# Optimization experiments

Hardware: AMD Instinct MI355X
Metric: run time of the kernel (lower is better)

## Reference

```python
import jax, jax.numpy as jnp
import numpy as np

N_NODES = 50000
N_EDGES = 800000
HIDDEN = 128
OUT = 10
N_LAYERS = 2
N_GRAPHS = 128
EPS = 1e-5


def setup_inputs() -> dict:
    key = jax.random.key(0)
    ks = jax.random.split(key, 10)
    x = jax.random.normal(ks[0], (N_NODES, HIDDEN), dtype=jnp.float32)
    edge_index = jax.random.randint(ks[1], (2, N_EDGES), 0, N_NODES, dtype=jnp.int64)
    batch = jnp.sort(jax.random.randint(ks[2], (N_NODES,), 0, N_GRAPHS, dtype=jnp.int64))
    s = 1.0 / np.sqrt(HIDDEN)
    # GraphConv params per layer: lin_rel (weight+bias, applied to aggregated neighbors)
    # and lin_root (weight, applied to the node itself). LayerNorm gamma/beta per layer.
    W_rel = jax.random.uniform(ks[3], (N_LAYERS, HIDDEN, HIDDEN), jnp.float32, -s, s)
    b_rel = jax.random.uniform(ks[4], (N_LAYERS, HIDDEN), jnp.float32, -s, s)
    W_root = jax.random.uniform(ks[5], (N_LAYERS, HIDDEN, HIDDEN), jnp.float32, -s, s)
    gamma = jnp.ones((N_LAYERS, HIDDEN), jnp.float32)
    beta = jnp.zeros((N_LAYERS, HIDDEN), jnp.float32)
    Wc = jax.random.uniform(ks[6], (HIDDEN, OUT), jnp.float32, -s, s)
    bc = jax.random.uniform(ks[7], (OUT,), jnp.float32, -s, s)
    return {"x": x, "edge_index": edge_index, "batch": batch,
            "W_rel": W_rel, "b_rel": b_rel, "W_root": W_root,
            "gamma": gamma, "beta": beta, "Wc": Wc, "bc": bc}


def _layer_norm(x, g, b):
    mu = jnp.mean(x, axis=-1, keepdims=True)
    var = jnp.mean(jnp.square(x - mu), axis=-1, keepdims=True)
    return g * (x - mu) * jax.lax.rsqrt(var + EPS) + b


def reference(x, edge_index, batch, W_rel, b_rel, W_root, gamma, beta, Wc, bc):
    src, dst = edge_index[0], edge_index[1]
    n = x.shape[0]
    # in-degree for mean aggregation (PyG: zero rows for isolated nodes)
    deg = jax.ops.segment_sum(jnp.ones((src.shape[0],), x.dtype), dst, num_segments=n)
    inv_deg = jnp.where(deg > 0, 1.0 / jnp.maximum(deg, 1.0), 0.0)[:, None]
    for l in range(N_LAYERS):
        agg = jax.ops.segment_sum(x[src], dst, num_segments=n) * inv_deg  # [N, H]
        x = agg @ W_rel[l] + b_rel[l] + x @ W_root[l]
        x = _layer_norm(x, gamma[l], beta[l])
        x = jax.nn.relu(x)
        # feat_dropout = 0.0 -> identity
    cnt = jax.ops.segment_sum(jnp.ones((n,), x.dtype), batch, num_segments=N_GRAPHS)
    pooled = jax.ops.segment_sum(x, batch, num_segments=N_GRAPHS)
    pooled = pooled / jnp.maximum(cnt, 1.0)[:, None]  # [G, H]
    return pooled @ Wc + bc
```

## Files before the change

### kernel.cpp

```cpp
#include <hip/hip_runtime.h>
#include <hip/hip_bf16.h>

#define N_NODES 50000
#define N_EDGES 800000
#define HIDDEN  128
#define OUT_F   10
#define N_GRAPHS 128
#define EPS 1e-5f

#define NB   391
#define BCAP 3072
#define SLICE (N_EDGES / 256)

#define CASTX_BLOCKS 12500
#define CASTW_BLOCKS 256
#define POOLZ_BLOCKS 64

using short8 = __attribute__((ext_vector_type(8))) short;
using f32x4  = __attribute__((ext_vector_type(4))) float;

__global__ void cast_zero_kernel(const float* __restrict__ x, __hip_bfloat16* __restrict__ xb,
                                 const float* __restrict__ Wrel, const float* __restrict__ Wroot,
                                 __hip_bfloat16* __restrict__ Wt,
                                 int* __restrict__ cursor, float* __restrict__ pooled) {
    const int b = blockIdx.x, tid = threadIdx.x;
    if (b < CASTX_BLOCKS) {
        int i = b * 256 + tid;
        float2 v = ((const float2*)x)[i];
        __hip_bfloat162 o;
        o.x = __float2bfloat16(v.x);
        o.y = __float2bfloat16(v.y);
        ((__hip_bfloat162*)xb)[i] = o;
    } else if (b < CASTX_BLOCKS + CASTW_BLOCKS) {
        int idx = (b - CASTX_BLOCKS) * 256 + tid;
        int l = idx >> 15;
        int rem = idx & 32767;
        int n = rem >> 8;
        int k = rem & 255;
        float v = (k < HIDDEN) ? Wrel[l * HIDDEN * HIDDEN + k * HIDDEN + n]
                               : Wroot[l * HIDDEN * HIDDEN + (k - HIDDEN) * HIDDEN + n];
        Wt[idx] = __float2bfloat16(v);
    } else if (b < CASTX_BLOCKS + CASTW_BLOCKS + POOLZ_BLOCKS) {
        int i = (b - CASTX_BLOCKS - CASTW_BLOCKS) * 256 + tid;
        pooled[i] = 0.f;
    } else {
        for (int i = tid; i < NB; i += 256) cursor[i] = 0;
    }
}

__global__ __launch_bounds__(256) void part_kernel(
        const int* __restrict__ src, const int* __restrict__ dst,
        int* __restrict__ cursor, int* __restrict__ ebuf) {
    __shared__ int s_pk[SLICE];
    __shared__ unsigned short s_bk[SLICE];
    __shared__ int hist[NB], base[NB];
    const int tid = threadIdx.x;
    const int e0 = blockIdx.x * SLICE;
    for (int i = tid; i < NB; i += 256) hist[i] = 0;
    __syncthreads();
    for (int i = tid; i < SLICE; i += 256) {
        int s = src[e0 + i], d = dst[e0 + i];
        int b = d >> 7;
        s_pk[i] = s | ((d & 127) << 16);
        s_bk[i] = (unsigned short)b;
        atomicAdd(&hist[b], 1);
    }
    __syncthreads();
    for (int i = tid; i < NB; i += 256) {
        int h = hist[i];
        base[i] = h ? atomicAdd(&cursor[i], h) : 0;
        hist[i] = 0;
    }
    __syncthreads();
    for (int i = tid; i < SLICE; i += 256) {
        int b = s_bk[i];
        int off = base[b] + atomicAdd(&hist[b], 1);
        if (off < BCAP) ebuf[b * BCAP + off] = s_pk[i];
    }
}

__global__ __launch_bounds__(256) void fillb_kernel(
        const int* __restrict__ cursor, const int* __restrict__ ebuf,
        int* __restrict__ row_ptr, float* __restrict__ inv_deg,
        int* __restrict__ csr_src) {
    __shared__ int lcsr[BCAP];
    __shared__ int hist[128], lofs[128];
    __shared__ int wtot[2];
    __shared__ int sred[4];
    __shared__ int sbase;
    const int b = blockIdx.x;
    const int tid = threadIdx.x;

    int partial = 0;
    for (int i = tid; i < b; i += 256) partial += cursor[i];
    #pragma unroll
    for (int off = 1; off < 64; off <<= 1) partial += __shfl_xor(partial, off, 64);
    if ((tid & 63) == 0) sred[tid >> 6] = partial;
    if (tid < 128) hist[tid] = 0;
    __syncthreads();
    if (tid == 0) sbase = sred[0] + sred[1] + sred[2] + sred[3];
    __syncthreads();
    const int base = sbase;

    int cnt = cursor[b]; if (cnt > BCAP) cnt = BCAP;
    const int* eb = ebuf + b * BCAP;

    for (int i = tid; i < cnt; i += 256) atomicAdd(&hist[eb[i] >> 16], 1);
    __syncthreads();
    if (tid < 128) {
        int lane = tid & 63;
        int v = hist[tid];
        int inc = v;
        #pragma unroll
        for (int off = 1; off < 64; off <<= 1) {
            int t = __shfl_up(inc, off, 64);
            if (lane >= off) inc += t;
        }
        lofs[tid] = inc - v;
        if (lane == 63) wtot[tid >> 6] = inc;
    }
    __syncthreads();
    if (tid >= 64 && tid < 128) lofs[tid] += wtot[0];
    __syncthreads();
    if (tid < 128) {
        int node = b * 128 + tid;
        if (node < N_NODES) {
            row_ptr[node] = base + lofs[tid];
            int d = hist[tid];
            inv_deg[node] = (d > 0) ? (1.0f / (float)d) : 0.0f;
        }
        hist[tid] = lofs[tid];
    }
    if (b == 0 && tid == 0) row_ptr[N_NODES] = N_EDGES;
    __syncthreads();
    for (int i = tid; i < cnt; i += 256) {
        int pk = eb[i];
        int p = atomicAdd(&hist[pk >> 16], 1);
        lcsr[p] = pk & 0xFFFF;
    }
    __syncthreads();
    for (int i = tid; i < cnt; i += 256) csr_src[base + i] = lcsr[i];
}

__global__ void agg_kernel(const __hip_bfloat16* __restrict__ x, const int* __restrict__ row_ptr,
                           const int* __restrict__ csr_src, const float* __restrict__ inv_deg,
                           __hip_bfloat16* __restrict__ agg) {
    int gid = blockIdx.x * blockDim.x + threadIdx.x;
    int node = gid >> 6;
    int lane = threadIdx.x & 63;
    if (node >= N_NODES) return;
    const int half = lane >> 5;
    const int l32  = lane & 31;
    const int beg = row_ptr[node], end = row_ptr[node + 1];

    float a[4][4];
    #pragma unroll
    for (int u = 0; u < 4; ++u)
        #pragma unroll
        for (int k = 0; k < 4; ++k) a[u][k] = 0.f;

    for (int c = beg; c < end; c += 64) {
        int ei = c + lane;
        int sidx = (ei < end) ? csr_src[ei] : 0;
        int nedge = end - c; if (nedge > 64) nedge = 64;
        int npair = nedge >> 1;
        int j = 0;
        for (; j + 4 <= npair; j += 4) {
            #pragma unroll
            for (int u = 0; u < 4; ++u) {
                int sj = __shfl(sidx, 2 * (j + u) + half, 64);
                float2 v = ((const float2*)(x + (size_t)sj * HIDDEN))[l32];
                __hip_bfloat162 b0 = *(__hip_bfloat162*)&v.x;
                __hip_bfloat162 b1 = *(__hip_bfloat162*)&v.y;
                a[u][0] += __bfloat162float(b0.x);
                a[u][1] += __bfloat162float(b0.y);
                a[u][2] += __bfloat162float(b1.x);
                a[u][3] += __bfloat162float(b1.y);
            }
        }
        for (; j < npair; ++j) {
            int sj = __shfl(sidx, 2 * j + half, 64);
            float2 v = ((const float2*)(x + (size_t)sj * HIDDEN))[l32];
            __hip_bfloat162 b0 = *(__hip_bfloat162*)&v.x;
            __hip_bfloat162 b1 = *(__hip_bfloat162*)&v.y;
            a[0][0] += __bfloat162float(b0.x);
            a[0][1] += __bfloat162float(b0.y);
            a[0][2] += __bfloat162float(b1.x);
            a[0][3] += __bfloat162float(b1.y);
        }
        if (nedge & 1) {
            int sj = __shfl(sidx, nedge - 1, 64);
            if (half == 0) {
                float2 v = ((const float2*)(x + (size_t)sj * HIDDEN))[l32];
                __hip_bfloat162 b0 = *(__hip_bfloat162*)&v.x;
                __hip_bfloat162 b1 = *(__hip_bfloat162*)&v.y;
                a[0][0] += __bfloat162float(b0.x);
                a[0][1] += __bfloat162float(b0.y);
                a[0][2] += __bfloat162float(b1.x);
                a[0][3] += __bfloat162float(b1.y);
            }
        }
    }

    float s0 = a[0][0] + a[1][0] + a[2][0] + a[3][0];
    float s1 = a[0][1] + a[1][1] + a[2][1] + a[3][1];
    float s2 = a[0][2] + a[1][2] + a[2][2] + a[3][2];
    float s3 = a[0][3] + a[1][3] + a[2][3] + a[3][3];
    s0 += __shfl_xor(s0, 32, 64);
    s1 += __shfl_xor(s1, 32, 64);
    s2 += __shfl_xor(s2, 32, 64);
    s3 += __shfl_xor(s3, 32, 64);

    if (half == 0) {
        float w = inv_deg[node];
        __hip_bfloat162 p0, p1;
        p0.x = __float2bfloat16(s0 * w);
        p0.y = __float2bfloat16(s1 * w);
        p1.x = __float2bfloat16(s2 * w);
        p1.y = __float2bfloat16(s3 * w);
        __hip_bfloat162* op = (__hip_bfloat162*)agg + (size_t)node * 64 + l32 * 2;
        op[0] = p0;
        op[1] = p1;
    }
}

#define GM 64

__global__ __launch_bounds__(256) void gemm_mfma_ln_kernel(
        const __hip_bfloat16* __restrict__ aggb, const __hip_bfloat16* __restrict__ xb,
        __hip_bfloat16* __restrict__ xout,
        const __hip_bfloat16* __restrict__ Wt,
        const float* __restrict__ brel, const float* __restrict__ gamma,
        const float* __restrict__ beta) {
    __shared__ __align__(16) short sA[GM * 264];
    __shared__ float red[GM][4][2];

    const int tid  = threadIdx.x;
    const int w    = tid >> 6;
    const int lane = tid & 63;
    const int q    = lane >> 4;
    const int l15  = lane & 15;
    const int base = blockIdx.x * GM;

    short8 breg[2][8];
    #pragma unroll
    for (int nt = 0; nt < 2; ++nt) {
        int col = 32 * w + nt * 16 + l15;
        const short* wp = (const short*)Wt + (size_t)col * 256;
        #pragma unroll
        for (int ks = 0; ks < 8; ++ks)
            breg[nt][ks] = *(const short8*)(wp + ks * 32 + q * 8);
    }

    for (int it = 0; it < 8; ++it) {
        int c = it * 256 + tid;
        int row = c >> 5, cc = c & 31;
        int node = base + row;
        short8 v = {0,0,0,0,0,0,0,0};
        if (node < N_NODES) {
            const short* gp = (cc < 16)
                ? (const short*)aggb + (size_t)node * HIDDEN + cc * 8
                : (const short*)xb   + (size_t)node * HIDDEN + (cc - 16) * 8;
            v = *(const short8*)gp;
        }
        *(short8*)&sA[row * 264 + cc * 8] = v;
    }
    __syncthreads();

    f32x4 acc[4][2];
    #pragma unroll
    for (int mt = 0; mt < 4; ++mt)
        #pragma unroll
        for (int nt = 0; nt < 2; ++nt)
            acc[mt][nt] = (f32x4){0.f, 0.f, 0.f, 0.f};

    #pragma unroll
    for (int ks = 0; ks < 8; ++ks) {
        short8 a[4];
        #pragma unroll
        for (int mt = 0; mt < 4; ++mt)
            a[mt] = *(short8*)&sA[(mt * 16 + l15) * 264 + ks * 32 + q * 8];
        #pragma unroll
        for (int mt = 0; mt < 4; ++mt) {
            acc[mt][0] = __builtin_amdgcn_mfma_f32_16x16x32_bf16(a[mt], breg[0][ks], acc[mt][0], 0, 0, 0);
            acc[mt][1] = __builtin_amdgcn_mfma_f32_16x16x32_bf16(a[mt], breg[1][ks], acc[mt][1], 0, 0, 0);
        }
    }

    const int col0 = 32 * w + l15, col1 = col0 + 16;
    const float b0 = brel[col0], b1 = brel[col1];
    #pragma unroll
    for (int mt = 0; mt < 4; ++mt) {
        #pragma unroll
        for (int r = 0; r < 4; ++r) {
            acc[mt][0][r] += b0;
            acc[mt][1][r] += b1;
            float s  = acc[mt][0][r] + acc[mt][1][r];
            float s2 = acc[mt][0][r] * acc[mt][0][r] + acc[mt][1][r] * acc[mt][1][r];
            #pragma unroll
            for (int off = 1; off < 16; off <<= 1) {
                s  += __shfl_xor(s,  off, 64);
                s2 += __shfl_xor(s2, off, 64);
            }
            if (l15 == 0) {
                red[mt * 16 + q * 4 + r][w][0] = s;
                red[mt * 16 + q * 4 + r][w][1] = s2;
            }
        }
    }
    __syncthreads();

    const float g0 = gamma[col0], g1 = gamma[col1];
    const float e0 = beta[col0],  e1 = beta[col1];
    #pragma unroll
    for (int mt = 0; mt < 4; ++mt) {
        #pragma unroll
        for (int r = 0; r < 4; ++r) {
            int row = mt * 16 + q * 4 + r;
            float tot  = red[row][0][0] + red[row][1][0] + red[row][2][0] + red[row][3][0];
            float tot2 = red[row][0][1] + red[row][1][1] + red[row][2][1] + red[row][3][1];
            float mu  = tot * (1.0f / HIDDEN);
            float var = tot2 * (1.0f / HIDDEN) - mu * mu;
            float rs  = rsqrtf(var + EPS);
            int node = base + row;
            if (node < N_NODES) {
                float v0 = fmaxf(g0 * (acc[mt][0][r] - mu) * rs + e0, 0.f);
                float v1 = fmaxf(g1 * (acc[mt][1][r] - mu) * rs + e1, 0.f);
                xout[(size_t)node * HIDDEN + col0] = __float2bfloat16(v0);
                xout[(size_t)node * HIDDEN + col1] = __float2bfloat16(v1);
            }
        }
    }
}

__global__ __launch_bounds__(256) void gemm_mfma_pool_kernel(
        const __hip_bfloat16* __restrict__ aggb, const __hip_bfloat16* __restrict__ xb,
        const int* __restrict__ batch, float* __restrict__ pooled,
        const __hip_bfloat16* __restrict__ Wt,
        const float* __restrict__ brel, const float* __restrict__ gamma,
        const float* __restrict__ beta) {
    __shared__ __align__(16) short sA[GM * 264];
    __shared__ float red[GM][4][2];
    __shared__ int sbatch[GM];

    const int tid  = threadIdx.x;
    const int w    = tid >> 6;
    const int lane = tid & 63;
    const int q    = lane >> 4;
    const int l15  = lane & 15;
    const int base = blockIdx.x * GM;

    if (tid < GM) {
        int node = base + tid;
        sbatch[tid] = (node < N_NODES) ? batch[node] : -1;
    }

    short8 breg[2][8];
    #pragma unroll
    for (int nt = 0; nt < 2; ++nt) {
        int col = 32 * w + nt * 16 + l15;
        const short* wp = (const short*)Wt + (size_t)col * 256;
        #pragma unroll
        for (int ks = 0; ks < 8; ++ks)
            breg[nt][ks] = *(const short8*)(wp + ks * 32 + q * 8);
    }

    for (int it = 0; it < 8; ++it) {
        int c = it * 256 + tid;
        int row = c >> 5, cc = c & 31;
        int node = base + row;
        short8 v = {0,0,0,0,0,0,0,0};
        if (node < N_NODES) {
            const short* gp = (cc < 16)
                ? (const short*)aggb + (size_t)node * HIDDEN + cc * 8
                : (const short*)xb   + (size_t)node * HIDDEN + (cc - 16) * 8;
            v = *(const short8*)gp;
        }
        *(short8*)&sA[row * 264 + cc * 8] = v;
    }
    __syncthreads();

    f32x4 acc[4][2];
    #pragma unroll
    for (int mt = 0; mt < 4; ++mt)
        #pragma unroll
        for (int nt = 0; nt < 2; ++nt)
            acc[mt][nt] = (f32x4){0.f, 0.f, 0.f, 0.f};

    #pragma unroll
    for (int ks = 0; ks < 8; ++ks) {
        short8 a[4];
        #pragma unroll
        for (int mt = 0; mt < 4; ++mt)
            a[mt] = *(short8*)&sA[(mt * 16 + l15) * 264 + ks * 32 + q * 8];
        #pragma unroll
        for (int mt = 0; mt < 4; ++mt) {
            acc[mt][0] = __builtin_amdgcn_mfma_f32_16x16x32_bf16(a[mt], breg[0][ks], acc[mt][0], 0, 0, 0);
            acc[mt][1] = __builtin_amdgcn_mfma_f32_16x16x32_bf16(a[mt], breg[1][ks], acc[mt][1], 0, 0, 0);
        }
    }

    const int col0 = 32 * w + l15, col1 = col0 + 16;
    const float b0 = brel[col0], b1 = brel[col1];
    #pragma unroll
    for (int mt = 0; mt < 4; ++mt) {
        #pragma unroll
        for (int r = 0; r < 4; ++r) {
            acc[mt][0][r] += b0;
            acc[mt][1][r] += b1;
            float s  = acc[mt][0][r] + acc[mt][1][r];
            float s2 = acc[mt][0][r] * acc[mt][0][r] + acc[mt][1][r] * acc[mt][1][r];
            #pragma unroll
            for (int off = 1; off < 16; off <<= 1) {
                s  += __shfl_xor(s,  off, 64);
                s2 += __shfl_xor(s2, off, 64);
            }
            if (l15 == 0) {
                red[mt * 16 + q * 4 + r][w][0] = s;
                red[mt * 16 + q * 4 + r][w][1] = s2;
            }
        }
    }
    __syncthreads();

    const float g0 = gamma[col0], g1 = gamma[col1];
    const float e0 = beta[col0],  e1 = beta[col1];
    #pragma unroll
    for (int mt = 0; mt < 4; ++mt) {
        #pragma unroll
        for (int r = 0; r < 4; ++r) {
            int row = mt * 16 + q * 4 + r;
            float tot  = red[row][0][0] + red[row][1][0] + red[row][2][0] + red[row][3][0];
            float tot2 = red[row][0][1] + red[row][1][1] + red[row][2][1] + red[row][3][1];
            float mu  = tot * (1.0f / HIDDEN);
            float var = tot2 * (1.0f / HIDDEN) - mu * mu;
            float rs  = rsqrtf(var + EPS);
            bool valid = (base + row) < N_NODES;
            float v0 = valid ? fmaxf(g0 * (acc[mt][0][r] - mu) * rs + e0, 0.f) : 0.f;
            float v1 = valid ? fmaxf(g1 * (acc[mt][1][r] - mu) * rs + e1, 0.f) : 0.f;
            acc[mt][0][r] = v0;
            acc[mt][1][r] = v1;
        }
    }

    int idxmax = N_NODES - 1 - base; if (idxmax > GM - 1) idxmax = GM - 1;
    const int gmin = sbatch[0], gmax = sbatch[idxmax];
    for (int g = gmin; g <= gmax; ++g) {
        float p0 = 0.f, p1 = 0.f;
        #pragma unroll
        for (int mt = 0; mt < 4; ++mt) {
            #pragma unroll
            for (int r = 0; r < 4; ++r) {
                int row = mt * 16 + q * 4 + r;
                if (sbatch[row] == g) { p0 += acc[mt][0][r]; p1 += acc[mt][1][r]; }
            }
        }
        p0 += __shfl_xor(p0, 16, 64); p0 += __shfl_xor(p0, 32, 64);
        p1 += __shfl_xor(p1, 16, 64); p1 += __shfl_xor(p1, 32, 64);
        if (q == 0) {
            atomicAdd(&pooled[g * HIDDEN + col0], p0);
            atomicAdd(&pooled[g * HIDDEN + col1], p1);
        }
    }
}

__global__ void out_kernel(const float* __restrict__ pooled, const int* __restrict__ batch,
                           const float* __restrict__ Wc, const float* __restrict__ bc,
                           float* __restrict__ out) {
    int idx = blockIdx.x * blockDim.x + threadIdx.x;
    if (idx >= N_GRAPHS * OUT_F) return;
    int g = idx / OUT_F, o = idx % OUT_F;
    int lo = 0, hi = N_NODES;
    while (lo < hi) { int m = (lo + hi) >> 1; if (batch[m] < g) lo = m + 1; else hi = m; }
    int b0 = lo;
    lo = 0; hi = N_NODES;
    while (lo < hi) { int m = (lo + hi) >> 1; if (batch[m] < g + 1) lo = m + 1; else hi = m; }
    float cntf = (float)(lo - b0);
    float inv = 1.0f / fmaxf(cntf, 1.0f);
    float s = 0.f;
    for (int f = 0; f < HIDDEN; ++f)
        s += pooled[g * HIDDEN + f] * Wc[f * OUT_F + o];
    out[idx] = s * inv + bc[o];
}

static inline size_t align256(size_t v) { return (v + 255) & ~(size_t)255; }

extern "C" void kernel_launch(void* const* d_in, const int* in_sizes, int n_in,
                              void* d_out, int out_size, void* d_ws, size_t ws_size,
                              hipStream_t stream) {
    const float* x      = (const float*)d_in[0];
    const int*   eidx   = (const int*)d_in[1];
    const int*   batch  = (const int*)d_in[2];
    const float* W_rel  = (const float*)d_in[3];
    const float* b_rel  = (const float*)d_in[4];
    const float* W_root = (const float*)d_in[5];
    const float* gamma  = (const float*)d_in[6];
    const float* beta   = (const float*)d_in[7];
    const float* Wc     = (const float*)d_in[8];
    const float* bc     = (const float*)d_in[9];
    float* out = (float*)d_out;

    const int* src = eidx;
    const int* dst = eidx + N_EDGES;

    char* ws = (char*)d_ws;
    size_t off = 0;
    int*   row_ptr  = (int*)(ws + off);  off = align256(off + sizeof(int) * (N_NODES + 1));
    int*   csr_src  = (int*)(ws + off);  off = align256(off + sizeof(int) * N_EDGES);
    float* inv_deg  = (float*)(ws + off); off = align256(off + sizeof(float) * N_NODES);
    int*   cursor   = (int*)(ws + off);  off = align256(off + sizeof(int) * NB);
    int*   ebuf     = (int*)(ws + off);  off = align256(off + sizeof(int) * (size_t)NB * BCAP);
    __hip_bfloat16* x0b  = (__hip_bfloat16*)(ws + off); off = align256(off + 2 * (size_t)N_NODES * HIDDEN);
    __hip_bfloat16* x1b  = (__hip_bfloat16*)(ws + off); off = align256(off + 2 * (size_t)N_NODES * HIDDEN);
    __hip_bfloat16* aggb = (__hip_bfloat16*)(ws + off); off = align256(off + 2 * (size_t)N_NODES * HIDDEN);
    __hip_bfloat16* Wt   = (__hip_bfloat16*)(ws + off); off = align256(off + 2 * (size_t)2 * HIDDEN * 256);
    float* pooled   = (float*)(ws + off); off = align256(off + sizeof(float) * N_GRAPHS * HIDDEN);

    cast_zero_kernel<<<CASTX_BLOCKS + CASTW_BLOCKS + POOLZ_BLOCKS + 1, 256, 0, stream>>>(
        x, x0b, W_rel, W_root, Wt, cursor, pooled);

    part_kernel <<<256, 256, 0, stream>>>(src, dst, cursor, ebuf);
    fillb_kernel<<<NB, 256, 0, stream>>>(cursor, ebuf, row_ptr, inv_deg, csr_src);

    const int agg_blocks  = (N_NODES * 64) / 256;
    const int gemm_blocks = (N_NODES + GM - 1) / GM;

    agg_kernel<<<agg_blocks, 256, 0, stream>>>(x0b, row_ptr, csr_src, inv_deg, aggb);
    gemm_mfma_ln_kernel<<<gemm_blocks, 256, 0, stream>>>(
        aggb, x0b, x1b, Wt, b_rel, gamma, beta);
    agg_kernel<<<agg_blocks, 256, 0, stream>>>(x1b, row_ptr, csr_src, inv_deg, aggb);
    gemm_mfma_pool_kernel<<<gemm_blocks, 256, 0, stream>>>(
        aggb, x1b, batch, pooled, Wt + 2 * HIDDEN * 256 / 2,
        b_rel + HIDDEN, gamma + HIDDEN, beta + HIDDEN);

    out_kernel<<<(N_GRAPHS * OUT_F + 255) / 256, 256, 0, stream>>>(pooled, batch, Wc, bc, out);
}
```

Measured before the change: 229.9 us.

## Gather neighbor features in FP8 and merge partition into prep kernel

Adds FP8 (e4m3) copies of the node features, written by the cast kernel and by the layer-1 LayerNorm epilogue. The aggregation kernels gather these instead of the bf16 rows, halving the bytes read per edge in the memory-bound gather. Separately, the edge-partition kernel is merged into the cast/prep launch, and the cursor is zeroed with a memset. The FP8 path loses precision in the aggregated features, which may hurt accuracy tolerance, and the extra byte-wise FP8 stores add write traffic to the GEMM epilogue.

```diff
diff --git a/kernel.cpp b/kernel.cpp
--- a/kernel.cpp
+++ b/kernel.cpp
@@ -1,5 +1,6 @@
 #include <hip/hip_runtime.h>
 #include <hip/hip_bf16.h>
+#include <hip/hip_fp8.h>
 
 #define N_NODES 50000
 #define N_EDGES 800000
@@ -12,27 +13,88 @@
 #define BCAP 3072
 #define SLICE (N_EDGES / 256)
 
-#define CASTX_BLOCKS 12500
-#define CASTW_BLOCKS 256
-#define POOLZ_BLOCKS 64
+#define PART_B0   0
+#define CASTW_B0  256
+#define POOLZ_B0  512
+#define CASTX_B0  576
+#define CASTX_NB  6250
+#define PREP_NB   (CASTX_B0 + CASTX_NB)
 
 using short8 = __attribute__((ext_vector_type(8))) short;
 using f32x4  = __attribute__((ext_vector_type(4))) float;
 
-__global__ void cast_zero_kernel(const float* __restrict__ x, __hip_bfloat16* __restrict__ xb,
-                                 const float* __restrict__ Wrel, const float* __restrict__ Wroot,
-                                 __hip_bfloat16* __restrict__ Wt,
-                                 int* __restrict__ cursor, float* __restrict__ pooled) {
+__device__ __forceinline__ unsigned int f4_to_fp8x4(float a, float b, float c, float d) {
+#if __has_builtin(__builtin_amdgcn_cvt_pk_fp8_f32)
+    int v = 0;
+    v = __builtin_amdgcn_cvt_pk_fp8_f32(a, b, v, false);
+    v = __builtin_amdgcn_cvt_pk_fp8_f32(c, d, v, true);
+    return (unsigned int)v;
+#else
+    __hip_fp8_e4m3 ha(a), hb(b), hc(c), hd(d);
+    return (unsigned int)ha.__x | ((unsigned int)hb.__x << 8) |
+           ((unsigned int)hc.__x << 16) | ((unsigned int)hd.__x << 24);
+#endif
+}
+__device__ __forceinline__ unsigned char f_to_fp8(float a) {
+#if __has_builtin(__builtin_amdgcn_cvt_pk_fp8_f32)
+    return (unsigned char)(__builtin_amdgcn_cvt_pk_fp8_f32(a, a, 0, false) & 0xff);
+#else
+    __hip_fp8_e4m3 h(a); return h.__x;
+#endif
+}
+__device__ __forceinline__ void fp8x4_to_f(unsigned int w, float o[4]) {
+#if __has_builtin(__builtin_amdgcn_cvt_pk_f32_fp8)
+    typedef float v2f __attribute__((ext_vector_type(2)));
+    v2f lo = __builtin_amdgcn_cvt_pk_f32_fp8((int)w, false);
+    v2f hi = __builtin_amdgcn_cvt_pk_f32_fp8((int)w, true);
+    o[0] = lo.x; o[1] = lo.y; o[2] = hi.x; o[3] = hi.y;
+#else
+    #pragma unroll
+    for (int t = 0; t < 4; ++t) {
+        __hip_fp8_e4m3 h; h.__x = (unsigned char)((w >> (8 * t)) & 0xff);
+        o[t] = (float)h;
+    }
+#endif
+}
+
+__global__ __launch_bounds__(256) void prep_kernel(
+        const float* __restrict__ x, __hip_bfloat16* __restrict__ x0b,
+        unsigned char* __restrict__ x0f,
+        const float* __restrict__ Wrel, const float* __restrict__ Wroot,
+        __hip_bfloat16* __restrict__ Wt,
+        const int* __restrict__ src, const int* __restrict__ dst,
+        int* __restrict__ cursor, int* __restrict__ ebuf,
+        float* __restrict__ pooled) {
+    __shared__ int s_pk[SLICE];
+    __shared__ unsigned short s_bk[SLICE];
+    __shared__ int hist[NB], base[NB];
     const int b = blockIdx.x, tid = threadIdx.x;
-    if (b < CASTX_BLOCKS) {
-        int i = b * 256 + tid;
-        float2 v = ((const float2*)x)[i];
-        __hip_bfloat162 o;
-        o.x = __float2bfloat16(v.x);
-        o.y = __float2bfloat16(v.y);
-        ((__hip_bfloat162*)xb)[i] = o;
-    } else if (b < CASTX_BLOCKS + CASTW_BLOCKS) {
-        int idx = (b - CASTX_BLOCKS) * 256 + tid;
+
+    if (b < CASTW_B0) {
+        const int e0 = b * SLICE;
+        for (int i = tid; i < NB; i += 256) hist[i] = 0;
+        __syncthreads();
+        for (int i = tid; i < SLICE; i += 256) {
+            int s = src[e0 + i], d = dst[e0 + i];
+            int bk = d >> 7;
+            s_pk[i] = s | ((d & 127) << 16);
+            s_bk[i] = (unsigned short)bk;
+            atomicAdd(&hist[bk], 1);
+        }
+        __syncthreads();
+        for (int i = tid; i < NB; i += 256) {
+            int h = hist[i];
+            base[i] = h ? atomicAdd(&cursor[i], h) : 0;
+            hist[i] = 0;
+        }
+        __syncthreads();
+        for (int i = tid; i < SLICE; i += 256) {
+            int bk = s_bk[i];
+            int off = base[bk] + atomicAdd(&hist[bk], 1);
+            if (off < BCAP) ebuf[bk * BCAP + off] = s_pk[i];
+        }
+    } else if (b < POOLZ_B0) {
+        int idx = (b - CASTW_B0) * 256 + tid;
         int l = idx >> 15;
         int rem = idx & 32767;
         int n = rem >> 8;
@@ -40,42 +102,19 @@
         float v = (k < HIDDEN) ? Wrel[l * HIDDEN * HIDDEN + k * HIDDEN + n]
                                : Wroot[l * HIDDEN * HIDDEN + (k - HIDDEN) * HIDDEN + n];
         Wt[idx] = __float2bfloat16(v);
-    } else if (b < CASTX_BLOCKS + CASTW_BLOCKS + POOLZ_BLOCKS) {
-        int i = (b - CASTX_BLOCKS - CASTW_BLOCKS) * 256 + tid;
+    } else if (b < CASTX_B0) {
+        int i = (b - POOLZ_B0) * 256 + tid;
         pooled[i] = 0.f;
     } else {
-        for (int i = tid; i < NB; i += 256) cursor[i] = 0;
-    }
-}
-
-__global__ __launch_bounds__(256) void part_kernel(
-        const int* __restrict__ src, const int* __restrict__ dst,
-        int* __restrict__ cursor, int* __restrict__ ebuf) {
-    __shared__ int s_pk[SLICE];
-    __shared__ unsigned short s_bk[SLICE];
-    __shared__ int hist[NB], base[NB];
-    const int tid = threadIdx.x;
-    const int e0 = blockIdx.x * SLICE;
-    for (int i = tid; i < NB; i += 256) hist[i] = 0;
-    __syncthreads();
-    for (int i = tid; i < SLICE; i += 256) {
-        int s = src[e0 + i], d = dst[e0 + i];
-        int b = d >> 7;
-        s_pk[i] = s | ((d & 127) << 16);
-        s_bk[i] = (unsigned short)b;
-        atomicAdd(&hist[b], 1);
-    }
-    __syncthreads();
-    for (int i = tid; i < NB; i += 256) {
-        int h = hist[i];
-        base[i] = h ? atomicAdd(&cursor[i], h) : 0;
-        hist[i] = 0;
-    }
-    __syncthreads();
-    for (int i = tid; i < SLICE; i += 256) {
-        int b = s_bk[i];
-        int off = base[b] + atomicAdd(&hist[b], 1);
-        if (off < BCAP) ebuf[b * BCAP + off] = s_pk[i];
+        int i = (b - CASTX_B0) * 256 + tid;
+        float4 v = ((const float4*)x)[i];
+        union { __hip_bfloat162 h[2]; uint2 u; } o;
+        o.h[0].x = __float2bfloat16(v.x);
+        o.h[0].y = __float2bfloat16(v.y);
+        o.h[1].x = __float2bfloat16(v.z);
+        o.h[1].y = __float2bfloat16(v.w);
+        ((uint2*)x0b)[i] = o.u;
+        ((unsigned int*)x0f)[i] = f4_to_fp8x4(v.x, v.y, v.z, v.w);
     }
 }
 
@@ -142,7 +181,7 @@
     for (int i = tid; i < cnt; i += 256) csr_src[base + i] = lcsr[i];
 }
 
-__global__ void agg_kernel(const __hip_bfloat16* __restrict__ x, const int* __restrict__ row_ptr,
+__global__ void agg_kernel(const unsigned char* __restrict__ xf8, const int* __restrict__ row_ptr,
                            const int* __restrict__ csr_src, const float* __restrict__ inv_deg,
                            __hip_bfloat16* __restrict__ agg) {
     int gid = blockIdx.x * blockDim.x + threadIdx.x;
@@ -169,35 +208,26 @@
             #pragma unroll
             for (int u = 0; u < 4; ++u) {
                 int sj = __shfl(sidx, 2 * (j + u) + half, 64);
-                float2 v = ((const float2*)(x + (size_t)sj * HIDDEN))[l32];
-                __hip_bfloat162 b0 = *(__hip_bfloat162*)&v.x;
-                __hip_bfloat162 b1 = *(__hip_bfloat162*)&v.y;
-                a[u][0] += __bfloat162float(b0.x);
-                a[u][1] += __bfloat162float(b0.y);
-                a[u][2] += __bfloat162float(b1.x);
-                a[u][3] += __bfloat162float(b1.y);
+                unsigned int wv = ((const unsigned int*)(xf8 + (size_t)sj * HIDDEN))[l32];
+                float f[4];
+                fp8x4_to_f(wv, f);
+                a[u][0] += f[0]; a[u][1] += f[1]; a[u][2] += f[2]; a[u][3] += f[3];
             }
         }
         for (; j < npair; ++j) {
             int sj = __shfl(sidx, 2 * j + half, 64);
-            float2 v = ((const float2*)(x + (size_t)sj * HIDDEN))[l32];
-            __hip_bfloat162 b0 = *(__hip_bfloat162*)&v.x;
-            __hip_bfloat162 b1 = *(__hip_bfloat162*)&v.y;
-            a[0][0] += __bfloat162float(b0.x);
-            a[0][1] += __bfloat162float(b0.y);
-            a[0][2] += __bfloat162float(b1.x);
-            a[0][3] += __bfloat162float(b1.y);
+            unsigned int wv = ((const unsigned int*)(xf8 + (size_t)sj * HIDDEN))[l32];
+            float f[4];
+            fp8x4_to_f(wv, f);
+            a[0][0] += f[0]; a[0][1] += f[1]; a[0][2] += f[2]; a[0][3] += f[3];
         }
         if (nedge & 1) {
             int sj = __shfl(sidx, nedge - 1, 64);
             if (half == 0) {
-                float2 v = ((const float2*)(x + (size_t)sj * HIDDEN))[l32];
-                __hip_bfloat162 b0 = *(__hip_bfloat162*)&v.x;
-                __hip_bfloat162 b1 = *(__hip_bfloat162*)&v.y;
-                a[0][0] += __bfloat162float(b0.x);
-                a[0][1] += __bfloat162float(b0.y);
-                a[0][2] += __bfloat162float(b1.x);
-                a[0][3] += __bfloat162float(b1.y);
+                unsigned int wv = ((const unsigned int*)(xf8 + (size_t)sj * HIDDEN))[l32];
+                float f[4];
+                fp8x4_to_f(wv, f);
+                a[0][0] += f[0]; a[0][1] += f[1]; a[0][2] += f[2]; a[0][3] += f[3];
             }
         }
     }
@@ -228,7 +258,7 @@
 
 __global__ __launch_bounds__(256) void gemm_mfma_ln_kernel(
         const __hip_bfloat16* __restrict__ aggb, const __hip_bfloat16* __restrict__ xb,
-        __hip_bfloat16* __restrict__ xout,
+        __hip_bfloat16* __restrict__ xout, unsigned char* __restrict__ xoutf,
         const __hip_bfloat16* __restrict__ Wt,
         const float* __restrict__ brel, const float* __restrict__ gamma,
         const float* __restrict__ beta) {
@@ -328,6 +358,8 @@
                 float v1 = fmaxf(g1 * (acc[mt][1][r] - mu) * rs + e1, 0.f);
                 xout[(size_t)node * HIDDEN + col0] = __float2bfloat16(v0);
                 xout[(size_t)node * HIDDEN + col1] = __float2bfloat16(v1);
+                xoutf[(size_t)node * HIDDEN + col0] = f_to_fp8(v0);
+                xoutf[(size_t)node * HIDDEN + col1] = f_to_fp8(v1);
             }
         }
     }
@@ -513,22 +545,24 @@
     __hip_bfloat16* x0b  = (__hip_bfloat16*)(ws + off); off = align256(off + 2 * (size_t)N_NODES * HIDDEN);
     __hip_bfloat16* x1b  = (__hip_bfloat16*)(ws + off); off = align256(off + 2 * (size_t)N_NODES * HIDDEN);
     __hip_bfloat16* aggb = (__hip_bfloat16*)(ws + off); off = align256(off + 2 * (size_t)N_NODES * HIDDEN);
+    unsigned char* x0f = (unsigned char*)(ws + off); off = align256(off + (size_t)N_NODES * HIDDEN);
+    unsigned char* x1f = (unsigned char*)(ws + off); off = align256(off + (size_t)N_NODES * HIDDEN);
     __hip_bfloat16* Wt   = (__hip_bfloat16*)(ws + off); off = align256(off + 2 * (size_t)2 * HIDDEN * 256);
     float* pooled   = (float*)(ws + off); off = align256(off + sizeof(float) * N_GRAPHS * HIDDEN);
 
-    cast_zero_kernel<<<CASTX_BLOCKS + CASTW_BLOCKS + POOLZ_BLOCKS + 1, 256, 0, stream>>>(
-        x, x0b, W_rel, W_root, Wt, cursor, pooled);
-
-    part_kernel <<<256, 256, 0, stream>>>(src, dst, cursor, ebuf);
+    hipMemsetAsync(cursor, 0, sizeof(int) * NB, stream);
+
+    prep_kernel<<<PREP_NB, 256, 0, stream>>>(
+        x, x0b, x0f, W_rel, W_root, Wt, src, dst, cursor, ebuf, pooled);
     fillb_kernel<<<NB, 256, 0, stream>>>(cursor, ebuf, row_ptr, inv_deg, csr_src);
 
     const int agg_blocks  = (N_NODES * 64) / 256;
     const int gemm_blocks = (N_NODES + GM - 1) / GM;
 
-    agg_kernel<<<agg_blocks, 256, 0, stream>>>(x0b, row_ptr, csr_src, inv_deg, aggb);
+    agg_kernel<<<agg_blocks, 256, 0, stream>>>(x0f, row_ptr, csr_src, inv_deg, aggb);
     gemm_mfma_ln_kernel<<<gemm_blocks, 256, 0, stream>>>(
-        aggb, x0b, x1b, Wt, b_rel, gamma, beta);
-    agg_kernel<<<agg_blocks, 256, 0, stream>>>(x1b, row_ptr, csr_src, inv_deg, aggb);
+        aggb, x0b, x1b, x1f, Wt, b_rel, gamma, beta);
+    agg_kernel<<<agg_blocks, 256, 0, stream>>>(x1f, row_ptr, csr_src, inv_deg, aggb);
     gemm_mfma_pool_kernel<<<gemm_blocks, 256, 0, stream>>>(
         aggb, x1b, batch, pooled, Wt + 2 * HIDDEN * 256 / 2,
         b_rel + HIDDEN, gamma + HIDDEN, beta + HIDDEN);
```

After: 216.5 us. 5.8% less time.
